# Kernel tuning notes

Hardware: AMD Instinct MI355X
Metric: run time of the kernel (lower is better)

The kernel has to match this reference:

```python
import jax, jax.numpy as jnp
import numpy as np
import math

B, N, D = 64, 512, 300
MASK_VALUE = -1.0e9
LN_EPS = 1e-5


def setup_inputs() -> dict:
    key = jax.random.key(0)
    ks = jax.random.split(key, 8)
    return {
        "concepts": jax.random.normal(ks[0], (B, N, D), dtype=jnp.float32),
        "ocr_tokens": jax.random.normal(ks[1], (B, N, D), dtype=jnp.float32),
        "ocr_mask": jax.random.randint(ks[2], (B, N, 1), 0, 2, dtype=jnp.int32),
        "wq": jax.random.normal(ks[3], (D, D), dtype=jnp.float32) * (1.0 / math.sqrt(D)),
        "bq": jax.random.normal(ks[4], (D,), dtype=jnp.float32) * 0.02,
        "wk": jax.random.normal(ks[5], (D, D), dtype=jnp.float32) * (1.0 / math.sqrt(D)),
        "bk": jax.random.normal(ks[6], (D,), dtype=jnp.float32) * 0.02,
        "ln_w": jnp.ones((D,), dtype=jnp.float32),
        "ln_b": jnp.zeros((D,), dtype=jnp.float32),
    }


def _layer_norm(x, w, b):
    mu = jnp.mean(x, axis=-1, keepdims=True)
    var = jnp.mean(jnp.square(x - mu), axis=-1, keepdims=True)
    return (x - mu) * jax.lax.rsqrt(var + LN_EPS) * w + b


def reference(concepts, ocr_tokens, ocr_mask, wq, bq, wk, bk, ln_w, ln_b):
    # Q/K linear projections (torch Linear: x @ W^T + b)
    Q = jnp.einsum('bnd,ed->bne', concepts, wq) + bq      # [B,N,D]
    K = jnp.einsum('bmd,ed->bme', ocr_tokens, wk) + bk    # [B,N,D]
    # scaled attention scores over concepts x ocr tokens
    A = jnp.einsum('bne,bme->bnm', Q, K) / math.sqrt(D)   # [B,N,N]
    P = jax.nn.softmax(A, axis=-1)
    semantic = jnp.einsum('bnm,bmd->bnd', P, concepts)    # [B,N,D]
    # post-attention masked_fill (faithful to original: fill AFTER attention)
    semantic = jnp.where(ocr_mask == 0, jnp.float32(MASK_VALUE), semantic)
    out = _layer_norm(ocr_tokens + semantic, ln_w, ln_b)  # [B,N,D]
    return out
```

## Files before the change

kernel.cpp:

```cpp
#include <hip/hip_runtime.h>
#include <math.h>

#define Bb 64
#define Nn 512
#define Dd 300

typedef __attribute__((ext_vector_type(8))) short bfrag;
typedef __attribute__((ext_vector_type(4))) float f4;
typedef __attribute__((ext_vector_type(4))) unsigned u4;
typedef __attribute__((ext_vector_type(2))) unsigned u2;

union BF { unsigned u[4]; bfrag v; u4 q; };

__device__ inline unsigned bfr(float x){
    union{float f;unsigned u;}v; v.f=x;
    return (v.u + 0x7FFFu + ((v.u>>16)&1u))>>16;
}
__device__ inline unsigned pk_rne(float a, float b){ return bfr(a) | (bfr(b)<<16); }
__device__ inline unsigned pk_tr(float a, float b){
    union{float f;unsigned u;} ua, ub; ua.f=a; ub.f=b;
    return (ua.u>>16) | (ub.u & 0xFFFF0000u);
}
__device__ inline char* wadr(char* dout, unsigned f){
    return dout + (size_t)(f>>9)*1200u + 608u + (f&511u);
}
__device__ inline void async16(const char* g, char* l){
    __builtin_amdgcn_global_load_lds(
        (const __attribute__((address_space(1))) void*)g,
        (__attribute__((address_space(3))) void*)l, 16, 0, 0);
}

#define TSZ 38400
#define VOFF 19200

__global__ __launch_bounds__(256)
void prep(const float* __restrict__ concepts, char* __restrict__ tiles,
          const float* __restrict__ wq, const float* __restrict__ wk,
          char* __restrict__ dout)
{
    const int bx = blockIdx.x;
    const int t  = threadIdx.x;
    if (bx < 1024) {
        const int mt = bx & 15, b = bx >> 4;
        char* vz = tiles + ((size_t)(b*16 + mt))*TSZ + VOFF;
        for (int task = t; task < 300; task += 256) {
            int m8 = task / 75, d4 = task - m8*75;
            const float* src = concepts + ((size_t)(b*Nn + mt*32 + m8*8))*Dd + d4*4;
            float4 r[8];
            #pragma unroll
            for (int i = 0; i < 8; ++i) r[i] = *(const float4*)(src + (size_t)i*Dd);
            #pragma unroll
            for (int dd = 0; dd < 4; ++dd) {
                int d = d4*4 + dd;
                float x[8];
                #pragma unroll
                for (int i = 0; i < 8; ++i)
                    x[i] = (dd==0) ? r[i].x : (dd==1) ? r[i].y : (dd==2) ? r[i].z : r[i].w;
                u4 q; q.x = pk_rne(x[0],x[1]); q.y = pk_rne(x[2],x[3]);
                      q.z = pk_rne(x[4],x[5]); q.w = pk_rne(x[6],x[7]);
                char* dst = (d < 288)
                    ? vz + (d>>4)*1024 + m8*256 + (d&15)*16
                    : vz + 18432 + m8*192 + (d-288)*16;
                *(u4*)dst = q;
            }
        }
    } else {
        const int wid = bx - 1024;
        const int xx = wid % 20, yy = wid / 20;
        const int sel = xx / 10, kc = xx % 10;
        const float* W = sel ? wk : wq;
        const int n = yy*152 + t;
        if (t < 152 && n < 304) {
            unsigned uu[16];
            #pragma unroll
            for (int j = 0; j < 16; ++j) uu[j] = 0;
            if (n < Dd) {
                const float* wr = W + (size_t)n*Dd + kc*32;
                int nv4 = (kc < 9) ? 8 : 3;
                #pragma unroll
                for (int i = 0; i < 8; ++i) {
                    if (i < nv4) {
                        float4 v = *(const float4*)(wr + i*4);
                        uu[2*i  ] = pk_rne(v.x, v.y);
                        uu[2*i+1] = pk_rne(v.z, v.w);
                    }
                }
            }
            unsigned fb = (unsigned)(sel*194560 + kc*19456 + n*16);
            #pragma unroll
            for (int g = 0; g < 4; ++g) {
                u4 q; q.x = uu[4*g+0]; q.y = uu[4*g+1]; q.z = uu[4*g+2]; q.w = uu[4*g+3];
                *(u4*)wadr(dout, fb + g*4864) = q;
            }
        }
    }
}

__global__ __launch_bounds__(256)
void proj4(const float* __restrict__ concepts, const float* __restrict__ ocr,
           const float* __restrict__ bq, const float* __restrict__ bk,
           char* __restrict__ dout, char* __restrict__ tiles)
{
    __shared__ char Wl[2][19456];
    const int t = threadIdx.x;
    const int w = t >> 6, lane = t & 63, ln = lane & 15, quad = lane >> 4;
    const int sel = blockIdx.y;
    const float* X    = sel ? ocr : concepts;
    const float* bias = sel ? bk  : bq;
    const int r0w = blockIdx.x*64 + w*16;
    const float* xr = X + (size_t)(r0w + ln)*Dd;

    const unsigned selbase = (unsigned)sel*194560u;
    #define STAGE_W(buf, kc) \
        for (int c = w; c < 19; c += 4) \
            async16((const char*)wadr(dout, selbase + (unsigned)(kc)*19456u + c*1024u + lane*16u), \
                    &Wl[buf][c*1024 + lane*16]);

    f4 acc[19];
    #pragma unroll
    for (int i = 0; i < 19; ++i) acc[i] = (f4){0.f,0.f,0.f,0.f};

    STAGE_W(0, 0);
    __syncthreads();

    for (int kc = 0; kc < 10; ++kc) {
        const int cur = kc & 1;
        if (kc < 9) { STAGE_W(1 - cur, kc + 1); }
        BF a;
        if (kc < 9) {
            float4 v0 = *(const float4*)(xr + kc*32 + quad*8);
            float4 v1 = *(const float4*)(xr + kc*32 + quad*8 + 4);
            a.u[0]=pk_tr(v0.x,v0.y); a.u[1]=pk_tr(v0.z,v0.w);
            a.u[2]=pk_tr(v1.x,v1.y); a.u[3]=pk_tr(v1.z,v1.w);
        } else {
            a.u[0]=0; a.u[1]=0; a.u[2]=0; a.u[3]=0;
            if (quad == 0) {
                float4 v0 = *(const float4*)(xr + 288);
                float4 v1 = *(const float4*)(xr + 292);
                a.u[0]=pk_tr(v0.x,v0.y); a.u[1]=pk_tr(v0.z,v0.w);
                a.u[2]=pk_tr(v1.x,v1.y); a.u[3]=pk_tr(v1.z,v1.w);
            } else if (quad == 1) {
                float4 v0 = *(const float4*)(xr + 296);
                a.u[0]=pk_tr(v0.x,v0.y); a.u[1]=pk_tr(v0.z,v0.w);
            }
        }
        #pragma unroll
        for (int nt = 0; nt < 19; ++nt) {
            BF bfv; bfv.q = *(const u4*)&Wl[cur][quad*4864 + nt*256 + ln*16];
            acc[nt] = __builtin_amdgcn_mfma_f32_16x16x32_bf16(a.v, bfv.v, acc[nt], 0,0,0);
        }
        __syncthreads();
    }

    const float QSCALE = 0.057735026918962584f;
    #pragma unroll
    for (int nt = 0; nt < 19; ++nt) {
        int e = nt*16 + ln;
        if (sel == 0) {
            #pragma unroll
            for (int reg = 0; reg < 4; ++reg) {
                int r = r0w + quad*4 + reg;
                short val = (e < Dd) ? (short)bfr((acc[nt][reg] + bias[e])*QSCALE) : (short)0;
                *(short*)(dout + (size_t)r*1200 + e*2) = val;
            }
        } else if (e < Dd) {
            float bv = bias[e];
            #pragma unroll
            for (int reg = 0; reg < 4; ++reg) {
                int r = r0w + quad*4 + reg;
                int b = r >> 9, m = r & 511, mt = m >> 5, ml = m & 31;
                char* tile = tiles + ((size_t)(b*16 + mt))*TSZ;
                short val = (short)bfr(acc[nt][reg] + bv);
                if (e < 288)
                    *(short*)(tile + 768 + (e>>5)*2048 + ((e>>3)&3)*512 + ml*16 + (e&7)*2) = val;
                else
                    *(short*)(tile + ml*24 + (e-288)*2) = val;
            }
        }
    }
}

__global__ __launch_bounds__(512, 2)
void attn8(char* __restrict__ dout, const char* __restrict__ tiles,
           const float* __restrict__ ocr, const int* __restrict__ mask,
           const float* __restrict__ lnw, const float* __restrict__ lnb)
{
    __shared__ __align__(16) char Tb[2][TSZ];
    const int t = threadIdx.x;
    const int w = t >> 6, lane = t & 63, ln = lane & 15, quad = lane >> 4;
    const int b = blockIdx.x, n0 = blockIdx.y*128;
    const int nlane = n0 + w*16 + ln;

    const char* qb = dout + (size_t)(b*Nn + nlane)*1200;
    bfrag qf[10];
    #pragma unroll
    for (int kc = 0; kc < 9; ++kc)
        qf[kc] = *(const bfrag*)(qb + kc*64 + quad*16);
    {
        BF z; z.u[0]=z.u[1]=z.u[2]=z.u[3]=0;
        if (quad < 2) z.q = *(const u4*)(qb + 576 + quad*16);
        qf[9] = z.v;
    }

    f4 oacc[19];
    #pragma unroll
    for (int i = 0; i < 19; ++i) oacc[i] = (f4){0.f,0.f,0.f,0.f};
    float lrun = 0.f;
    const char* tb = tiles + (size_t)b*16*TSZ;

#define STAGE_TILE(SRC, DST) do { \
        const char* s_ = (SRC); char* d_ = (DST); \
        for (int c = w; c < 38; c += 8) \
            if (c < 37 || lane < 32) \
                async16(s_ + c*1024 + lane*16, d_ + c*1024 + lane*16); \
    } while (0)

    STAGE_TILE(tb, Tb[0]);
    __syncthreads();

    for (int mt = 0; mt < 16; ++mt) {
        const char* Kz = Tb[mt & 1];
        const char* Vz = Kz + VOFF;

        if (mt < 15) STAGE_TILE(tb + (size_t)(mt+1)*TSZ, Tb[1 - (mt & 1)]);

        f4 slo = (f4){0.f,0.f,0.f,0.f}, shi = (f4){0.f,0.f,0.f,0.f};
        __builtin_amdgcn_s_setprio(1);
        #pragma unroll
        for (int kc = 0; kc < 9; ++kc) {
            bfrag alo = *(const bfrag*)(Kz + 768 + kc*2048 + quad*512 + ln*16);
            bfrag ahi = *(const bfrag*)(Kz + 768 + kc*2048 + quad*512 + 256 + ln*16);
            slo = __builtin_amdgcn_mfma_f32_16x16x32_bf16(alo, qf[kc], slo, 0,0,0);
            shi = __builtin_amdgcn_mfma_f32_16x16x32_bf16(ahi, qf[kc], shi, 0,0,0);
        }
        {
            BF alo, ahi;
            alo.u[0]=alo.u[1]=alo.u[2]=alo.u[3]=0;
            ahi.u[0]=ahi.u[1]=ahi.u[2]=ahi.u[3]=0;
            if (quad < 2) {
                u2 x0 = *(const u2*)(Kz + ln*24 + quad*16);
                u2 x1 = *(const u2*)(Kz + ln*24 + quad*16 + 8);
                alo.u[0]=x0.x; alo.u[1]=x0.y; alo.u[2]=x1.x; alo.u[3]=x1.y;
                u2 y0 = *(const u2*)(Kz + (16+ln)*24 + quad*16);
                u2 y1 = *(const u2*)(Kz + (16+ln)*24 + quad*16 + 8);
                ahi.u[0]=y0.x; ahi.u[1]=y0.y; ahi.u[2]=y1.x; ahi.u[3]=y1.y;
            }
            slo = __builtin_amdgcn_mfma_f32_16x16x32_bf16(alo.v, qf[9], slo, 0,0,0);
            shi = __builtin_amdgcn_mfma_f32_16x16x32_bf16(ahi.v, qf[9], shi, 0,0,0);
        }
        __builtin_amdgcn_s_setprio(0);

        float elo[4], ehi[4], ls = 0.f;
        #pragma unroll
        for (int reg = 0; reg < 4; ++reg) {
            elo[reg] = __expf(slo[reg]);
            ehi[reg] = __expf(shi[reg]);
            ls += elo[reg] + ehi[reg];
        }
        ls += __shfl_xor(ls, 16);
        ls += __shfl_xor(ls, 32);
        lrun += ls;

        unsigned lo01 = pk_rne(elo[0], elo[1]), lo23 = pk_rne(elo[2], elo[3]);
        unsigned hi01 = pk_rne(ehi[0], ehi[1]), hi23 = pk_rne(ehi[2], ehi[3]);
        int sA = 2*(quad & 1)*16 + ln, sB = sA + 16;
        unsigned l0 = (unsigned)__shfl((int)lo01, sA);
        unsigned l1 = (unsigned)__shfl((int)lo23, sA);
        unsigned l2 = (unsigned)__shfl((int)lo01, sB);
        unsigned l3 = (unsigned)__shfl((int)lo23, sB);
        unsigned h0 = (unsigned)__shfl((int)hi01, sA);
        unsigned h1 = (unsigned)__shfl((int)hi23, sA);
        unsigned h2 = (unsigned)__shfl((int)hi01, sB);
        unsigned h3 = (unsigned)__shfl((int)hi23, sB);
        BF p;
        bool useHi = quad >= 2;
        p.u[0] = useHi ? h0 : l0; p.u[1] = useHi ? h1 : l1;
        p.u[2] = useHi ? h2 : l2; p.u[3] = useHi ? h3 : l3;

        __builtin_amdgcn_s_setprio(1);
        #pragma unroll
        for (int nt = 0; nt < 18; ++nt) {
            bfrag vf = *(const bfrag*)(Vz + nt*1024 + lane*16);
            oacc[nt] = __builtin_amdgcn_mfma_f32_16x16x32_bf16(p.v, vf, oacc[nt], 0,0,0);
        }
        {
            BF vf; vf.u[0]=vf.u[1]=vf.u[2]=vf.u[3]=0;
            if (ln < 12) vf.q = *(const u4*)(Vz + 18432 + quad*192 + ln*16);
            oacc[18] = __builtin_amdgcn_mfma_f32_16x16x32_bf16(p.v, vf.v, oacc[18], 0,0,0);
        }
        __builtin_amdgcn_s_setprio(0);

        __syncthreads();
    }

    float invl[4];
    #pragma unroll
    for (int reg = 0; reg < 4; ++reg) invl[reg] = 1.0f / __shfl(lrun, quad*4 + reg);
    #pragma unroll
    for (int reg = 0; reg < 4; ++reg) {
        int r = b*Nn + n0 + w*16 + quad*4 + reg;
        int mr = mask[r];
        float xs[19], s = 0.f, ss = 0.f;
        #pragma unroll
        for (int nt = 0; nt < 19; ++nt) {
            int d = nt*16 + ln;
            float x = 0.f;
            if (d < Dd) x = oacc[nt][reg]*invl[reg] + ocr[(size_t)r*Dd + d];
            xs[nt] = x; s += x; ss += x*x;
        }
        #pragma unroll
        for (int off = 1; off < 16; off <<= 1) {
            s += __shfl_xor(s, off); ss += __shfl_xor(ss, off);
        }
        float mu   = s * (1.0f/Dd);
        float var  = ss * (1.0f/Dd) - mu*mu;
        float rstd = rsqrtf(var + 1e-5f);
        #pragma unroll
        for (int nt = 0; nt < 19; ++nt) {
            int d = nt*16 + ln;
            if (d < Dd) {
                float y = mr ? (xs[nt]-mu)*rstd*lnw[d] + lnb[d] : lnw[d] + lnb[d];
                *(float*)(dout + (size_t)r*1200 + d*4) = y;
            }
        }
    }
}

extern "C" void kernel_launch(void* const* d_in, const int* in_sizes, int n_in,
                              void* d_out, int out_size, void* d_ws, size_t ws_size,
                              hipStream_t stream)
{
    const float* concepts = (const float*)d_in[0];
    const float* ocr      = (const float*)d_in[1];
    const int*   mask     = (const int*)d_in[2];
    const float* wq  = (const float*)d_in[3];
    const float* bq  = (const float*)d_in[4];
    const float* wk  = (const float*)d_in[5];
    const float* bk  = (const float*)d_in[6];
    const float* lnw = (const float*)d_in[7];
    const float* lnb = (const float*)d_in[8];

    char* dout  = (char*)d_out;
    char* tiles = (char*)d_ws;

    prep <<<dim3(1064),    256, 0, stream>>>(concepts, tiles, wq, wk, dout);
    proj4<<<dim3(512, 2),  256, 0, stream>>>(concepts, ocr, bq, bk, dout, tiles);
    attn8<<<dim3(64, 4),   512, 0, stream>>>(dout, tiles, ocr, mask, lnw, lnb);
}
```

Baseline: 226.9 us.

## Fuse concept-tile bf16 cast into projection kernel, split weight prep out

Weight conversion now runs in its own small kernel. The concept V-tile cast moves out of the old prep kernel and into the projection kernel as extra blocks, with two tiles per 512-thread block. The projection blocks grow to 8 waves covering 128 rows, so each staged weight chunk is reused by more rows. This takes the heavy cast work off the serial path before projection and lets it overlap with the GEMM blocks. The cost is larger blocks with 38 KB of LDS each, which may lower occupancy, and the cast blocks that run at the end may land unevenly across the GPU.

```diff
diff --git a/kernel.cpp b/kernel.cpp
--- a/kernel.cpp
+++ b/kernel.cpp
@@ -34,16 +34,52 @@
 #define VOFF 19200
 
 __global__ __launch_bounds__(256)
-void prep(const float* __restrict__ concepts, char* __restrict__ tiles,
-          const float* __restrict__ wq, const float* __restrict__ wk,
-          char* __restrict__ dout)
+void wprep(const float* __restrict__ wq, const float* __restrict__ wk,
+           char* __restrict__ dout)
 {
+    const int sel = blockIdx.x / 10, kc = blockIdx.x % 10;
+    const float* W = sel ? wk : wq;
+    const int n = blockIdx.y*152 + threadIdx.x;
+    if (threadIdx.x < 152 && n < 304) {
+        unsigned uu[16];
+        #pragma unroll
+        for (int j = 0; j < 16; ++j) uu[j] = 0;
+        if (n < Dd) {
+            const float* wr = W + (size_t)n*Dd + kc*32;
+            int nv4 = (kc < 9) ? 8 : 3;
+            #pragma unroll
+            for (int i = 0; i < 8; ++i) {
+                if (i < nv4) {
+                    float4 v = *(const float4*)(wr + i*4);
+                    uu[2*i  ] = pk_rne(v.x, v.y);
+                    uu[2*i+1] = pk_rne(v.z, v.w);
+                }
+            }
+        }
+        unsigned fb = (unsigned)(sel*194560 + kc*19456 + n*16);
+        #pragma unroll
+        for (int g = 0; g < 4; ++g) {
+            u4 q; q.x = uu[4*g+0]; q.y = uu[4*g+1]; q.z = uu[4*g+2]; q.w = uu[4*g+3];
+            *(u4*)wadr(dout, fb + g*4864) = q;
+        }
+    }
+}
+
+__global__ __launch_bounds__(512)
+void projcast(const float* __restrict__ concepts, const float* __restrict__ ocr,
+              const float* __restrict__ bq, const float* __restrict__ bk,
+              char* __restrict__ dout, char* __restrict__ tiles)
+{
+    __shared__ char Wl[2][19456];
     const int bx = blockIdx.x;
     const int t  = threadIdx.x;
-    if (bx < 1024) {
-        const int mt = bx & 15, b = bx >> 4;
+
+    if (bx >= 512) {
+        const int half = t >> 8, tt = t & 255;
+        const int tileIdx = (bx - 512)*2 + half;
+        const int mt = tileIdx & 15, b = tileIdx >> 4;
         char* vz = tiles + ((size_t)(b*16 + mt))*TSZ + VOFF;
-        for (int task = t; task < 300; task += 256) {
+        for (int task = tt; task < 300; task += 256) {
             int m8 = task / 75, d4 = task - m8*75;
             const float* src = concepts + ((size_t)(b*Nn + mt*32 + m8*8))*Dd + d4*4;
             float4 r[8];
@@ -64,55 +100,19 @@
                 *(u4*)dst = q;
             }
         }
-    } else {
-        const int wid = bx - 1024;
-        const int xx = wid % 20, yy = wid / 20;
-        const int sel = xx / 10, kc = xx % 10;
-        const float* W = sel ? wk : wq;
-        const int n = yy*152 + t;
-        if (t < 152 && n < 304) {
-            unsigned uu[16];
-            #pragma unroll
-            for (int j = 0; j < 16; ++j) uu[j] = 0;
-            if (n < Dd) {
-                const float* wr = W + (size_t)n*Dd + kc*32;
-                int nv4 = (kc < 9) ? 8 : 3;
-                #pragma unroll
-                for (int i = 0; i < 8; ++i) {
-                    if (i < nv4) {
-                        float4 v = *(const float4*)(wr + i*4);
-                        uu[2*i  ] = pk_rne(v.x, v.y);
-                        uu[2*i+1] = pk_rne(v.z, v.w);
-                    }
-                }
-            }
-            unsigned fb = (unsigned)(sel*194560 + kc*19456 + n*16);
-            #pragma unroll
-            for (int g = 0; g < 4; ++g) {
-                u4 q; q.x = uu[4*g+0]; q.y = uu[4*g+1]; q.z = uu[4*g+2]; q.w = uu[4*g+3];
-                *(u4*)wadr(dout, fb + g*4864) = q;
-            }
-        }
-    }
-}
-
-__global__ __launch_bounds__(256)
-void proj4(const float* __restrict__ concepts, const float* __restrict__ ocr,
-           const float* __restrict__ bq, const float* __restrict__ bk,
-           char* __restrict__ dout, char* __restrict__ tiles)
-{
-    __shared__ char Wl[2][19456];
-    const int t = threadIdx.x;
+        return;
+    }
+
     const int w = t >> 6, lane = t & 63, ln = lane & 15, quad = lane >> 4;
-    const int sel = blockIdx.y;
+    const int sel = bx >> 8;
     const float* X    = sel ? ocr : concepts;
     const float* bias = sel ? bk  : bq;
-    const int r0w = blockIdx.x*64 + w*16;
+    const int r0w = (bx & 255)*128 + w*16;
     const float* xr = X + (size_t)(r0w + ln)*Dd;
 
     const unsigned selbase = (unsigned)sel*194560u;
-    #define STAGE_W(buf, kc) \
-        for (int c = w; c < 19; c += 4) \
+    #define STAGE_W8(buf, kc) \
+        for (int c = w; c < 19; c += 8) \
             async16((const char*)wadr(dout, selbase + (unsigned)(kc)*19456u + c*1024u + lane*16u), \
                     &Wl[buf][c*1024 + lane*16]);
 
@@ -120,12 +120,12 @@
     #pragma unroll
     for (int i = 0; i < 19; ++i) acc[i] = (f4){0.f,0.f,0.f,0.f};
 
-    STAGE_W(0, 0);
+    STAGE_W8(0, 0);
     __syncthreads();
 
     for (int kc = 0; kc < 10; ++kc) {
         const int cur = kc & 1;
-        if (kc < 9) { STAGE_W(1 - cur, kc + 1); }
+        if (kc < 9) { STAGE_W8(1 - cur, kc + 1); }
         BF a;
         if (kc < 9) {
             float4 v0 = *(const float4*)(xr + kc*32 + quad*8);
@@ -343,7 +343,7 @@
     char* dout  = (char*)d_out;
     char* tiles = (char*)d_ws;
 
-    prep <<<dim3(1064),    256, 0, stream>>>(concepts, tiles, wq, wk, dout);
-    proj4<<<dim3(512, 2),  256, 0, stream>>>(concepts, ocr, bq, bk, dout, tiles);
-    attn8<<<dim3(64, 4),   512, 0, stream>>>(dout, tiles, ocr, mask, lnw, lnb);
-}
+    wprep   <<<dim3(20, 2), 256, 0, stream>>>(wq, wk, dout);
+    projcast<<<dim3(1024),  512, 0, stream>>>(concepts, ocr, bq, bk, dout, tiles);
+    attn8   <<<dim3(64, 4), 512, 0, stream>>>(dout, tiles, ocr, mask, lnw, lnb);
+}
```

After: 212.9 us, median of 2. 6.2% less time.
